# Performance work log

Hardware: AMD Instinct MI355X
Metric: run time of the kernel (lower is better)

## Reference

```python
import jax, jax.numpy as jnp
import numpy as np

N, NFEAT, NHID, NREL, NCLASS, NHEADS = 4096, 512, 64, 64, 16, 8
ALPHA = 0.2   # LeakyReLU negative slope
NEG = -9e15   # pyGAT mask value


def _gat_layer(x, rel, mask, adj_ad, W, a1, a2, concat):
    # x: [N, Fin], rel: [nrel, Fin], mask: [N, N] bool, adj_ad: [N, nrel]
    xr = x + adj_ad @ rel                 # relation-augmented node features
    h = xr @ W                            # [N, Fout]
    f1 = h @ a1                           # [N]  (a^T[Wh_i||Wh_j] = f1_i + f2_j)
    f2 = h @ a2                           # [N]
    e = jax.nn.leaky_relu(f1[:, None] + f2[None, :], ALPHA)  # [N, N]
    att = jax.nn.softmax(jnp.where(mask, e, NEG), axis=1)
    out = att @ h                         # [N, Fout]
    return jax.nn.elu(out) if concat else out


def setup_inputs() -> dict:
    key = jax.random.key(0)
    ks = jax.random.split(key, 12)
    x = jax.random.normal(ks[0], (N, NFEAT), jnp.float32)
    rel = jax.random.normal(ks[1], (NREL, NFEAT), jnp.float32)
    rel_dict = jax.random.randint(ks[2], (N,), 0, NREL, jnp.int32)
    adj = (jax.random.uniform(ks[3], (N, N)) < 0.01).astype(jnp.float32)
    adj = jnp.maximum(adj, jnp.eye(N, dtype=jnp.float32))  # self loops
    adj_ad = jax.random.uniform(ks[4], (N, NREL), jnp.float32)
    adj_ad = adj_ad / adj_ad.sum(axis=1, keepdims=True)
    s_in = 1.0 / np.sqrt(NFEAT)
    s_hid = 1.0 / np.sqrt(NHID)
    s_cat = 1.0 / np.sqrt(NHID * NHEADS)
    W_heads = jax.random.normal(ks[5], (NHEADS, NFEAT, NHID), jnp.float32) * s_in
    a1_heads = jax.random.normal(ks[6], (NHEADS, NHID), jnp.float32) * s_hid
    a2_heads = jax.random.normal(ks[7], (NHEADS, NHID), jnp.float32) * s_hid
    W_out = jax.random.normal(ks[8], (NHID * NHEADS, NFEAT), jnp.float32) * s_cat
    a1_out = jax.random.normal(ks[9], (NFEAT,), jnp.float32) * s_in
    a2_out = jax.random.normal(ks[10], (NFEAT,), jnp.float32) * s_in
    lin_W = jax.random.normal(ks[11], (NFEAT, NCLASS), jnp.float32) * s_in
    lin_b = jnp.zeros((NCLASS,), jnp.float32)
    return {"x": x, "rel": rel, "rel_dict": rel_dict, "adj": adj, "adj_ad": adj_ad,
            "W_heads": W_heads, "a1_heads": a1_heads, "a2_heads": a2_heads,
            "W_out": W_out, "a1_out": a1_out, "a2_out": a2_out,
            "lin_W": lin_W, "lin_b": lin_b}


def reference(x, rel, rel_dict, adj, adj_ad, W_heads, a1_heads, a2_heads,
              W_out, a1_out, a2_out, lin_W, lin_b):
    # dropout is identity at inference (training=False); rel_dict is only used
    # by the repo to build adj/adj_ad, so it is a non-math constant here.
    mask = adj > 0
    # multi-head GAT layer, heads fused via vmap then concatenated on feature dim
    heads = jax.vmap(lambda W, a1, a2: _gat_layer(x, rel, mask, adj_ad, W, a1, a2, True))(
        W_heads, a1_heads, a2_heads)                      # [H, N, NHID]
    hcat = jnp.moveaxis(heads, 0, 1).reshape(N, NHEADS * NHID)  # [N, H*NHID]
    h2 = _gat_layer(hcat, rel, mask, adj_ad, W_out, a1_out, a2_out, False)  # [N, NFEAT]
    logits = jax.nn.elu(h2 @ lin_W + lin_b)               # [N, NCLASS]
    return jax.nn.log_softmax(logits, axis=1)
```

## Files before the change

### kernel.cpp

```cpp
#include <hip/hip_runtime.h>

#define NN      4096
#define FEAT    512
#define KDIM    576
#define NHID    64
#define NHEADS  8
#define NCLS    16
#define MAXDEG  128
#define ALPHA   0.2f

typedef __bf16 bf16_t;
typedef __bf16 bf16x8_t __attribute__((ext_vector_type(8)));
typedef float  f32x4_t  __attribute__((ext_vector_type(4)));
typedef unsigned short us8_t __attribute__((ext_vector_type(8)));

__device__ inline unsigned short f2bf(float f) {
    unsigned int u = __float_as_uint(f);
    u += 0x7fffu + ((u >> 16) & 1u);
    return (unsigned short)(u >> 16);
}
__device__ inline float bfu2f(unsigned short b) {
    return __uint_as_float(((unsigned int)b) << 16);
}
__device__ inline void gload16(const void* g, void* s) {
    __builtin_amdgcn_global_load_lds(
        (const __attribute__((address_space(1))) void*)g,
        (__attribute__((address_space(3))) void*)s, 16, 0, 0);
}

#define PREP_REL0   0
#define PREP_TR0    256
#define PREP_Z0     384
#define PREP_CAST0  520
#define PREP_CSR0   2568
#define PREP_NBLK   3592

__global__ __launch_bounds__(256) void prep_kernel(
    const float* __restrict__ adj, int* __restrict__ deg, int* __restrict__ cols,
    const float* __restrict__ adj_ad, const float* __restrict__ rel,
    const float* __restrict__ x, bf16_t* __restrict__ Abf,
    bf16_t* __restrict__ Abf2,
    const float* __restrict__ Wh, const float* __restrict__ Wo,
    unsigned short* __restrict__ WcT, unsigned short* __restrict__ WoT,
    float* __restrict__ fzero) {
    int b = blockIdx.x;
    int t = threadIdx.x;
    __shared__ float smem[64 * 65];
    if (b < PREP_TR0) {
        int r  = b & 63;
        int nh = (b >> 6) & 1;
        int n  = nh * 256 + t;
        smem[t]       = rel[r * FEAT + t];
        smem[t + 256] = rel[r * FEAT + 256 + t];
        __syncthreads();
        float acc[8] = {};
        if (b < 128) {
            int h = n >> 6, f = n & 63;
            const float* p = Wh + (size_t)h * 32768 + f;
            for (int k0 = 0; k0 < 512; k0 += 8)
                #pragma unroll
                for (int u = 0; u < 8; ++u)
                    acc[u] += smem[k0 + u] * p[(size_t)(k0 + u) * 64];
            float s = ((acc[0] + acc[1]) + (acc[2] + acc[3]))
                    + ((acc[4] + acc[5]) + (acc[6] + acc[7]));
            WcT[(size_t)n * KDIM + 512 + r] = f2bf(s);
        } else {
            const float* p = Wo + n;
            for (int k0 = 0; k0 < 512; k0 += 8)
                #pragma unroll
                for (int u = 0; u < 8; ++u)
                    acc[u] += smem[k0 + u] * p[(size_t)(k0 + u) * 512];
            float s = ((acc[0] + acc[1]) + (acc[2] + acc[3]))
                    + ((acc[4] + acc[5]) + (acc[6] + acc[7]));
            WoT[(size_t)n * KDIM + 512 + r] = f2bf(s);
        }
    } else if (b < PREP_Z0) {
        int tb = b - PREP_TR0;
        if (tb < 64) {
            int h = tb >> 3, k0 = (tb & 7) * 64;
            const float* src = Wh + (size_t)h * 32768 + (size_t)k0 * 64;
            #pragma unroll
            for (int i2 = 0; i2 < 16; ++i2) {
                int li = t + i2 * 256;
                float v = src[li];
                smem[(li & 63) * 65 + (li >> 6)] = v;
            }
            __syncthreads();
            #pragma unroll
            for (int i2 = 0; i2 < 16; ++i2) {
                int li = t + i2 * 256;
                int f = li >> 6, r = li & 63;
                WcT[(size_t)(h * 64 + f) * KDIM + k0 + r] = f2bf(smem[f * 65 + r]);
            }
        } else {
            int wb = tb - 64;
            int n0 = (wb & 7) * 64, k0 = (wb >> 3) * 64;
            #pragma unroll
            for (int i2 = 0; i2 < 16; ++i2) {
                int li = t + i2 * 256;
                int r = li >> 6, f = li & 63;
                float v = Wo[(size_t)(k0 + r) * 512 + n0 + f];
                smem[f * 65 + r] = v;
            }
            __syncthreads();
            #pragma unroll
            for (int i2 = 0; i2 < 16; ++i2) {
                int li = t + i2 * 256;
                int f = li >> 6, r = li & 63;
                WoT[(size_t)(n0 + f) * KDIM + k0 + r] = f2bf(smem[f * 65 + r]);
            }
        }
    } else if (b < PREP_CAST0) {
        int g = (b - PREP_Z0) * 256 + t;
        ((float4*)fzero)[g] = make_float4(0.f, 0.f, 0.f, 0.f);
    } else if (b < PREP_CSR0) {
        int half = t >> 7;
        int tt = t & 127;
        size_t i = (size_t)(b - PREP_CAST0) * 2 + half;
        float4 xv = ((const float4*)(x + i * FEAT))[tt];
        ushort4 o;
        o.x = f2bf(xv.x); o.y = f2bf(xv.y);
        o.z = f2bf(xv.z); o.w = f2bf(xv.w);
        *(ushort4*)(Abf + i * KDIM + 4 * tt) = o;
        if (tt < 16) {
            float4 av = ((const float4*)(adj_ad + i * 64))[tt];
            ushort4 o2;
            o2.x = f2bf(av.x); o2.y = f2bf(av.y);
            o2.z = f2bf(av.z); o2.w = f2bf(av.w);
            *(ushort4*)(Abf  + i * KDIM + 512 + 4 * tt) = o2;
            *(ushort4*)(Abf2 + i * KDIM + 512 + 4 * tt) = o2;
        }
    } else {
        int l = t & 63;
        int i = (b - PREP_CSR0) * 4 + (t >> 6);
        const float4* row4 = (const float4*)(adj + (size_t)i * NN);
        float4 v[16];
        #pragma unroll
        for (int c2 = 0; c2 < 16; ++c2) v[c2] = row4[l + c2 * 64];
        unsigned long long mask = 0;
        #pragma unroll
        for (int c2 = 0; c2 < 16; ++c2) {
            unsigned m4 = (unsigned)(v[c2].x > 0.0f)
                        | ((unsigned)(v[c2].y > 0.0f) << 1)
                        | ((unsigned)(v[c2].z > 0.0f) << 2)
                        | ((unsigned)(v[c2].w > 0.0f) << 3);
            mask |= (unsigned long long)m4 << (4 * c2);
        }
        int c = __popcll(mask);
        int pre = c;
        #pragma unroll
        for (int off = 1; off < 64; off <<= 1) {
            int n = __shfl_up(pre, off);
            if (l >= off) pre += n;
        }
        int base = pre - c;
        if (l == 63) deg[i] = pre > MAXDEG ? MAXDEG : pre;
        int* colrow = cols + i * MAXDEG;
        int idx = base;
        while (mask) {
            int bit = (int)__ffsll(mask) - 1;
            mask &= mask - 1;
            int j = 4 * l + ((bit >> 2) << 8) + (bit & 3);
            if (idx < MAXDEG) colrow[idx] = j;
            ++idx;
        }
    }
}

__global__ __launch_bounds__(256) void gemm_bf16_dot_kernel(
    const bf16_t* __restrict__ A, const bf16_t* __restrict__ Bt,
    unsigned short* __restrict__ Cbf,
    const float* __restrict__ a1, const float* __restrict__ a2,
    float* __restrict__ f1, float* __restrict__ f2, int layer2,
    const float* __restrict__ linW, float* __restrict__ G) {
    __shared__ __align__(16) bf16_t ABs[2][64][64];
    float* Ct = (float*)ABs;
    const int bm = blockIdx.x * 64;
    const int bn = blockIdx.y * 64;
    const int by = blockIdx.y;
    const int t  = threadIdx.x;
    const int l  = t & 63;
    const int w  = t >> 6;
    const int wr = w >> 1;
    const int wc = w & 1;
    const int c16 = l & 15;
    const int q8  = (l >> 4) * 8;
    const int r4  = (l >> 4) * 4;

    const bf16_t* Abase = A  + (size_t)bm * KDIM;
    const bf16_t* Bbase = Bt + (size_t)bn * KDIM;

    f32x4_t acc[2][2] = {};
    for (int k0 = 0; k0 < KDIM; k0 += 64) {
        #pragma unroll
        for (int c = 0; c < 2; ++c) {
            int cb = c * 256 + w * 64;
            int li = cb + l;
            int r = li >> 3, pc = li & 7;
            int lc = pc ^ (r & 7);
            gload16(Abase + (size_t)r * KDIM + k0 + lc * 8,
                    (char*)&ABs[0][0][0] + cb * 16);
        }
        #pragma unroll
        for (int c = 0; c < 2; ++c) {
            int cb = c * 256 + w * 64;
            int li = cb + l;
            int r = li >> 3, pc = li & 7;
            int lc = pc ^ (r & 7);
            gload16(Bbase + (size_t)r * KDIM + k0 + lc * 8,
                    (char*)&ABs[1][0][0] + cb * 16);
        }
        __syncthreads();
        #pragma unroll
        for (int kk = 0; kk < 64; kk += 32) {
            const int ck = (kk + q8) >> 3;
            bf16x8_t af[2], bfr[2];
            #pragma unroll
            for (int mi = 0; mi < 2; ++mi) {
                int R = wr * 32 + mi * 16 + c16;
                af[mi] = *(const bf16x8_t*)&ABs[0][R][(ck ^ (R & 7)) * 8];
            }
            #pragma unroll
            for (int ni = 0; ni < 2; ++ni) {
                int R = wc * 32 + ni * 16 + c16;
                bfr[ni] = *(const bf16x8_t*)&ABs[1][R][(ck ^ (R & 7)) * 8];
            }
            #pragma unroll
            for (int mi = 0; mi < 2; ++mi)
                #pragma unroll
                for (int ni = 0; ni < 2; ++ni)
                    acc[mi][ni] = __builtin_amdgcn_mfma_f32_16x16x32_bf16(
                        af[mi], bfr[ni], acc[mi][ni], 0, 0, 0);
        }
        __syncthreads();
    }
    if (layer2) {
        #pragma unroll
        for (int mi = 0; mi < 2; ++mi)
            #pragma unroll
            for (int ni = 0; ni < 2; ++ni)
                #pragma unroll
                for (int r = 0; r < 4; ++r)
                    Ct[(wr * 32 + mi * 16 + r4 + r) * 64
                       + wc * 32 + ni * 16 + c16] = acc[mi][ni][r];
    }
    #pragma unroll
    for (int mi = 0; mi < 2; ++mi)
        #pragma unroll
        for (int ni = 0; ni < 2; ++ni)
            #pragma unroll
            for (int r = 0; r < 4; ++r)
                Cbf[(size_t)(bm + wr * 32 + mi * 16 + r4 + r) * FEAT
                    + bn + wc * 32 + ni * 16 + c16] = f2bf(acc[mi][ni][r]);

    float a1v[2], a2v[2];
    #pragma unroll
    for (int ni = 0; ni < 2; ++ni) {
        a1v[ni] = a1[bn + wc * 32 + ni * 16 + c16];
        a2v[ni] = a2[bn + wc * 32 + ni * 16 + c16];
    }
    float p1[2][4] = {}, p2[2][4] = {};
    #pragma unroll
    for (int mi = 0; mi < 2; ++mi)
        #pragma unroll
        for (int ni = 0; ni < 2; ++ni)
            #pragma unroll
            for (int r = 0; r < 4; ++r) {
                p1[mi][r] += acc[mi][ni][r] * a1v[ni];
                p2[mi][r] += acc[mi][ni][r] * a2v[ni];
            }
    #pragma unroll
    for (int off = 1; off <= 8; off <<= 1)
        #pragma unroll
        for (int mi = 0; mi < 2; ++mi)
            #pragma unroll
            for (int r = 0; r < 4; ++r) {
                p1[mi][r] += __shfl_xor(p1[mi][r], off);
                p2[mi][r] += __shfl_xor(p2[mi][r], off);
            }
    if (c16 == 0) {
        int fbase = layer2 ? 0 : by * NN;
        #pragma unroll
        for (int mi = 0; mi < 2; ++mi)
            #pragma unroll
            for (int r = 0; r < 4; ++r) {
                int row = bm + wr * 32 + mi * 16 + r4 + r;
                atomicAdd(&f1[fbase + row], p1[mi][r]);
                atomicAdd(&f2[fbase + row], p2[mi][r]);
            }
    }
    if (layer2) {
        __syncthreads();
        int row = t >> 2;
        int cls0 = (t & 3) * 4;
        float pg[4] = {};
        #pragma unroll 8
        for (int c = 0; c < 64; ++c) {
            float cv = Ct[row * 64 + c];
            float4 wv = *(const float4*)&linW[(size_t)(bn + c) * NCLS + cls0];
            pg[0] += cv * wv.x; pg[1] += cv * wv.y;
            pg[2] += cv * wv.z; pg[3] += cv * wv.w;
        }
        #pragma unroll
        for (int j = 0; j < 4; ++j)
            atomicAdd(&G[(size_t)(bm + row) * NCLS + cls0 + j], pg[j]);
    }
}

__global__ __launch_bounds__(512) void att1_kernel(
    const bf16_t* __restrict__ Hbf, const float* __restrict__ f1,
    const float* __restrict__ f2, const int* __restrict__ deg,
    const int* __restrict__ cols, bf16_t* __restrict__ outbf) {
    int i = blockIdx.x;
    int tid = threadIdx.x;
    int h = tid >> 6;
    int l = tid & 63;
    __shared__ int jl[MAXDEG];
    __shared__ float se[NHEADS][MAXDEG];
    __shared__ float part[NHEADS][FEAT];
    __shared__ float sinv[NHEADS];
    __shared__ int sdeg;
    if (tid == 0) sdeg = deg[i];
    __syncthreads();
    int d = sdeg;
    int dpad = (d + 31) & ~31;
    for (int k = tid; k < dpad; k += 512)
        jl[k] = (k < d) ? cols[i * MAXDEG + k] : i;
    __syncthreads();
    float fi = f1[h * NN + i];
    float lmax = -1e30f;
    for (int k = l; k < d; k += 64) {
        float e = fi + f2[h * NN + jl[k]];
        e = e > 0.0f ? e : ALPHA * e;
        se[h][k] = e;
        lmax = fmaxf(lmax, e);
    }
    for (int off = 32; off; off >>= 1) lmax = fmaxf(lmax, __shfl_down(lmax, off));
    float m = __shfl(lmax, 0);
    float ls = 0.0f;
    for (int k = l; k < d; k += 64) {
        float p = __expf(se[h][k] - m);
        se[h][k] = p;
        ls += p;
    }
    for (int k = d + l; k < dpad; k += 64) se[h][k] = 0.0f;
    for (int off = 32; off; off >>= 1) ls += __shfl_down(ls, off);
    if (l == 0) sinv[h] = 1.0f / ls;
    __syncthreads();
    const int myhead = l >> 3;
    float acc[8] = {};
    for (int k0 = 0; k0 < dpad; k0 += 32) {
        float pw[4];
        const bf16_t* rp[4];
        #pragma unroll
        for (int j = 0; j < 4; ++j) {
            int k = k0 + j * 8 + h;
            pw[j] = se[myhead][k];
            rp[j] = Hbf + (size_t)jl[k] * FEAT + l * 8;
        }
        #pragma unroll
        for (int j = 0; j < 4; ++j) {
            us8_t v = *(const us8_t*)rp[j];
            float p = pw[j];
            #pragma unroll
            for (int q = 0; q < 8; ++q) acc[q] += p * bfu2f(v[q]);
        }
    }
    *(float4*)&part[h][l * 8]     = make_float4(acc[0], acc[1], acc[2], acc[3]);
    *(float4*)&part[h][l * 8 + 4] = make_float4(acc[4], acc[5], acc[6], acc[7]);
    __syncthreads();
    {
        float sum = 0.0f;
        #pragma unroll
        for (int w2 = 0; w2 < NHEADS; ++w2) sum += part[w2][tid];
        float o = sum * sinv[tid >> 6];
        o = o > 0.0f ? o : __expf(o) - 1.0f;
        ((unsigned short*)outbf)[(size_t)i * KDIM + tid] = f2bf(o);
    }
}

__global__ __launch_bounds__(256) void att2_final_kernel(
    const float* __restrict__ G, const float* __restrict__ f1,
    const float* __restrict__ f2, const int* __restrict__ deg,
    const int* __restrict__ cols, const float* __restrict__ linb,
    float* __restrict__ out) {
    int i = blockIdx.x;
    int t = threadIdx.x;
    __shared__ int jl[MAXDEG];
    __shared__ float sp[MAXDEG];
    __shared__ float red[4];
    __shared__ float clsred[16][NCLS];
    __shared__ float sl[NCLS];
    __shared__ int sdeg;
    if (t == 0) sdeg = deg[i];
    __syncthreads();
    int d = sdeg;
    int dpad = (d + 15) & ~15;
    if (t < dpad) jl[t] = (t < d) ? cols[i * MAXDEG + t] : i;
    __syncthreads();
    float e = 0.0f, lmax = -1e30f;
    if (t < d) {
        e = f1[i] + f2[jl[t]];
        e = e > 0.0f ? e : ALPHA * e;
        lmax = e;
    }
    for (int off = 32; off; off >>= 1) lmax = fmaxf(lmax, __shfl_down(lmax, off));
    if ((t & 63) == 0) red[t >> 6] = lmax;
    __syncthreads();
    float m = fmaxf(fmaxf(red[0], red[1]), fmaxf(red[2], red[3]));
    float p = 0.0f;
    if (t < d) p = __expf(e - m);
    if (t < dpad) sp[t] = p;
    float ls = p;
    for (int off = 32; off; off >>= 1) ls += __shfl_down(ls, off);
    __syncthreads();
    if ((t & 63) == 0) red[t >> 6] = ls;
    __syncthreads();
    float s = red[0] + red[1] + red[2] + red[3];
    float inv = 1.0f / s;
    {
        int slot = t >> 4;
        int cls  = t & 15;
        float fa[4] = {};
        for (int k = slot; k < dpad; k += 16)
            fa[(k >> 4) & 3] += sp[k] * G[(size_t)jl[k] * NCLS + cls];
        clsred[slot][cls] = (fa[0] + fa[1]) + (fa[2] + fa[3]);
    }
    __syncthreads();
    if (t < NCLS) {
        float dot = 0.0f;
        #pragma unroll
        for (int seg = 0; seg < 16; ++seg) dot += clsred[seg][t];
        float logit = linb[t] + dot * inv;
        logit = logit > 0.0f ? logit : __expf(logit) - 1.0f;
        sl[t] = logit;
    }
    __syncthreads();
    if (t < NCLS) {
        float mm = sl[0];
        #pragma unroll
        for (int c = 1; c < NCLS; ++c) mm = fmaxf(mm, sl[c]);
        float ssum = 0.0f;
        #pragma unroll
        for (int c = 0; c < NCLS; ++c) ssum += __expf(sl[c] - mm);
        out[i * NCLS + t] = sl[t] - mm - logf(ssum);
    }
}

extern "C" void kernel_launch(void* const* d_in, const int* in_sizes, int n_in,
                              void* d_out, int out_size, void* d_ws, size_t ws_size,
                              hipStream_t stream) {
    const float* x        = (const float*)d_in[0];
    const float* rel      = (const float*)d_in[1];
    const float* adj      = (const float*)d_in[3];
    const float* adj_ad   = (const float*)d_in[4];
    const float* W_heads  = (const float*)d_in[5];
    const float* a1_heads = (const float*)d_in[6];
    const float* a2_heads = (const float*)d_in[7];
    const float* W_out    = (const float*)d_in[8];
    const float* a1_out   = (const float*)d_in[9];
    const float* a2_out   = (const float*)d_in[10];
    const float* lin_W    = (const float*)d_in[11];
    const float* lin_b    = (const float*)d_in[12];
    float* out = (float*)d_out;

    char* ws = (char*)d_ws;
    bf16_t* Abf  = (bf16_t*)(ws);
    bf16_t* Abf2 = (bf16_t*)(ws + (5u  << 20));
    bf16_t* Hbf1 = (bf16_t*)(ws + (10u << 20));
    bf16_t* Hbf2 = (bf16_t*)(ws + (14u << 20));
    bf16_t* WcT  = (bf16_t*)(ws + (18u << 20));
    bf16_t* WoT  = (bf16_t*)(ws + (19u << 20));
    float*  f1   = (float*) (ws + (20u << 20));
    float*  f2   = (float*) (ws + (20u << 20) + (128u << 10));
    float*  f1o  = (float*) (ws + (20u << 20) + (256u << 10));
    float*  f2o  = (float*) (ws + (20u << 20) + (272u << 10));
    float*  G    = (float*) (ws + (20u << 20) + (288u << 10));
    int*    deg  = (int*)   (ws + (20u << 20) + (544u << 10));
    int*    cols = (int*)   (ws + (21u << 20));

    prep_kernel<<<PREP_NBLK, 256, 0, stream>>>(
        adj, deg, cols, adj_ad, rel, x, Abf, Abf2, W_heads, W_out,
        (unsigned short*)WcT, (unsigned short*)WoT, f1);
    gemm_bf16_dot_kernel<<<dim3(64, 8), 256, 0, stream>>>(
        Abf, WcT, (unsigned short*)Hbf1, a1_heads, a2_heads, f1, f2, 0,
        nullptr, nullptr);
    att1_kernel<<<NN, 512, 0, stream>>>(Hbf1, f1, f2, deg, cols, Abf2);
    gemm_bf16_dot_kernel<<<dim3(64, 8), 256, 0, stream>>>(
        Abf2, WoT, (unsigned short*)Hbf2, a1_out, a2_out, f1o, f2o, 1,
        lin_W, G);
    att2_final_kernel<<<NN, 256, 0, stream>>>(G, f1o, f2o, deg, cols, lin_b, out);
}
```

Measured before the change: 188.3 us.

## Fuse adjacency CSR construction into first attention kernel

Moves the dense adjacency scan that builds neighbor lists from the prep kernel into att1_kernel. Each attention block now reads its own adjacency row, builds the column list straight into shared memory with a two-level prefix scan, and writes deg/cols out for the later att2 kernel. This removes the global cols reads in att1 and shrinks prep's grid, but it puts the 64 MB adjacency read on att1's critical path and adds a block-wide sync at the start of att1. Column ordering changes from a per-wave interleaved layout to a per-thread-strided one, so neighbors end up in a different order.

Result: no change. 188.6 us (+0.2%).

```diff
diff --git a/kernel.cpp b/kernel.cpp
--- a/kernel.cpp
+++ b/kernel.cpp
@@ -32,11 +32,9 @@
 #define PREP_TR0    256
 #define PREP_Z0     384
 #define PREP_CAST0  520
-#define PREP_CSR0   2568
-#define PREP_NBLK   3592
+#define PREP_NBLK   2568
 
 __global__ __launch_bounds__(256) void prep_kernel(
-    const float* __restrict__ adj, int* __restrict__ deg, int* __restrict__ cols,
     const float* __restrict__ adj_ad, const float* __restrict__ rel,
     const float* __restrict__ x, bf16_t* __restrict__ Abf,
     bf16_t* __restrict__ Abf2,
@@ -113,7 +111,7 @@
     } else if (b < PREP_CAST0) {
         int g = (b - PREP_Z0) * 256 + t;
         ((float4*)fzero)[g] = make_float4(0.f, 0.f, 0.f, 0.f);
-    } else if (b < PREP_CSR0) {
+    } else {
         int half = t >> 7;
         int tt = t & 127;
         size_t i = (size_t)(b - PREP_CAST0) * 2 + half;
@@ -129,40 +127,6 @@
             o2.z = f2bf(av.z); o2.w = f2bf(av.w);
             *(ushort4*)(Abf  + i * KDIM + 512 + 4 * tt) = o2;
             *(ushort4*)(Abf2 + i * KDIM + 512 + 4 * tt) = o2;
-        }
-    } else {
-        int l = t & 63;
-        int i = (b - PREP_CSR0) * 4 + (t >> 6);
-        const float4* row4 = (const float4*)(adj + (size_t)i * NN);
-        float4 v[16];
-        #pragma unroll
-        for (int c2 = 0; c2 < 16; ++c2) v[c2] = row4[l + c2 * 64];
-        unsigned long long mask = 0;
-        #pragma unroll
-        for (int c2 = 0; c2 < 16; ++c2) {
-            unsigned m4 = (unsigned)(v[c2].x > 0.0f)
-                        | ((unsigned)(v[c2].y > 0.0f) << 1)
-                        | ((unsigned)(v[c2].z > 0.0f) << 2)
-                        | ((unsigned)(v[c2].w > 0.0f) << 3);
-            mask |= (unsigned long long)m4 << (4 * c2);
-        }
-        int c = __popcll(mask);
-        int pre = c;
-        #pragma unroll
-        for (int off = 1; off < 64; off <<= 1) {
-            int n = __shfl_up(pre, off);
-            if (l >= off) pre += n;
-        }
-        int base = pre - c;
-        if (l == 63) deg[i] = pre > MAXDEG ? MAXDEG : pre;
-        int* colrow = cols + i * MAXDEG;
-        int idx = base;
-        while (mask) {
-            int bit = (int)__ffsll(mask) - 1;
-            mask &= mask - 1;
-            int j = 4 * l + ((bit >> 2) << 8) + (bit & 3);
-            if (idx < MAXDEG) colrow[idx] = j;
-            ++idx;
         }
     }
 }
@@ -308,9 +272,9 @@
 }
 
 __global__ __launch_bounds__(512) void att1_kernel(
+    const float* __restrict__ adj, int* __restrict__ deg, int* __restrict__ cols,
     const bf16_t* __restrict__ Hbf, const float* __restrict__ f1,
-    const float* __restrict__ f2, const int* __restrict__ deg,
-    const int* __restrict__ cols, bf16_t* __restrict__ outbf) {
+    const float* __restrict__ f2, bf16_t* __restrict__ outbf) {
     int i = blockIdx.x;
     int tid = threadIdx.x;
     int h = tid >> 6;
@@ -319,14 +283,53 @@
     __shared__ float se[NHEADS][MAXDEG];
     __shared__ float part[NHEADS][FEAT];
     __shared__ float sinv[NHEADS];
+    __shared__ int wsum[8];
     __shared__ int sdeg;
-    if (tid == 0) sdeg = deg[i];
+    {
+        const float4* row4 = (const float4*)(adj + (size_t)i * NN);
+        float4 v0 = row4[tid];
+        float4 v1 = row4[tid + 512];
+        unsigned m = 0;
+        m |= (unsigned)(v0.x > 0.0f) << 0;  m |= (unsigned)(v0.y > 0.0f) << 1;
+        m |= (unsigned)(v0.z > 0.0f) << 2;  m |= (unsigned)(v0.w > 0.0f) << 3;
+        m |= (unsigned)(v1.x > 0.0f) << 4;  m |= (unsigned)(v1.y > 0.0f) << 5;
+        m |= (unsigned)(v1.z > 0.0f) << 6;  m |= (unsigned)(v1.w > 0.0f) << 7;
+        int c = __popc(m);
+        int pre = c;
+        #pragma unroll
+        for (int off = 1; off < 64; off <<= 1) {
+            int n = __shfl_up(pre, off);
+            if (l >= off) pre += n;
+        }
+        if (l == 63) wsum[h] = pre;
+        __syncthreads();
+        int base = pre - c;
+        #pragma unroll
+        for (int w2 = 0; w2 < 8; ++w2)
+            if (w2 < h) base += wsum[w2];
+        unsigned mm = m;
+        int idx = base;
+        while (mm) {
+            int bit = __ffs(mm) - 1;
+            mm &= mm - 1;
+            int j = 4 * tid + ((bit >> 2) << 11) + (bit & 3);
+            if (idx < MAXDEG) jl[idx] = j;
+            ++idx;
+        }
+        if (tid == 0) {
+            int tot = 0;
+            #pragma unroll
+            for (int w2 = 0; w2 < 8; ++w2) tot += wsum[w2];
+            tot = tot > MAXDEG ? MAXDEG : tot;
+            sdeg = tot;
+            deg[i] = tot;
+        }
+    }
     __syncthreads();
     int d = sdeg;
     int dpad = (d + 31) & ~31;
-    for (int k = tid; k < dpad; k += 512)
-        jl[k] = (k < d) ? cols[i * MAXDEG + k] : i;
-    __syncthreads();
+    for (int k = d + tid; k < dpad; k += 512) jl[k] = i;
+    for (int k = tid; k < d; k += 512) cols[i * MAXDEG + k] = jl[k];
     float fi = f1[h * NN + i];
     float lmax = -1e30f;
     for (int k = l; k < d; k += 64) {
@@ -480,12 +483,13 @@
     int*    cols = (int*)   (ws + (21u << 20));
 
     prep_kernel<<<PREP_NBLK, 256, 0, stream>>>(
-        adj, deg, cols, adj_ad, rel, x, Abf, Abf2, W_heads, W_out,
+        adj_ad, rel, x, Abf, Abf2, W_heads, W_out,
         (unsigned short*)WcT, (unsigned short*)WoT, f1);
     gemm_bf16_dot_kernel<<<dim3(64, 8), 256, 0, stream>>>(
         Abf, WcT, (unsigned short*)Hbf1, a1_heads, a2_heads, f1, f2, 0,
         nullptr, nullptr);
-    att1_kernel<<<NN, 512, 0, stream>>>(Hbf1, f1, f2, deg, cols, Abf2);
+    att1_kernel<<<NN, 512, 0, stream>>>(
+        adj, deg, cols, Hbf1, f1, f2, Abf2);
     gemm_bf16_dot_kernel<<<dim3(64, 8), 256, 0, stream>>>(
         Abf2, WoT, (unsigned short*)Hbf2, a1_out, a2_out, f1o, f2o, 1,
         lin_W, G);
```

## Move adjacency CSR build from prep kernel into first GEMM launch

Applied to the files above, without the earlier changes.

The dense-adjacency-to-CSR scan (reading the 64MB fp32 adj) moves out of the prep kernel and into extra blocks appended to the first GEMM launch, so the memory-bound scan can overlap with the compute-bound GEMM blocks. The GEMM grid becomes 1D with a manual block-index decode. The layer-2 GEMM also stops writing the unused bf16 H output. This makes the prep kernel shorter, at the cost of a more heterogeneous GEMM launch whose CSR blocks may compete with GEMM blocks for bandwidth and CUs.

Result: slower. 192.6 us (+2.3%).

```diff
diff --git a/kernel.cpp b/kernel.cpp
--- a/kernel.cpp
+++ b/kernel.cpp
@@ -9,6 +9,8 @@
 #define MAXDEG  128
 #define ALPHA   0.2f
 
+#define GEMM_BLKS 512
+
 typedef __bf16 bf16_t;
 typedef __bf16 bf16x8_t __attribute__((ext_vector_type(8)));
 typedef float  f32x4_t  __attribute__((ext_vector_type(4)));
@@ -32,11 +34,9 @@
 #define PREP_TR0    256
 #define PREP_Z0     384
 #define PREP_CAST0  520
-#define PREP_CSR0   2568
-#define PREP_NBLK   3592
+#define PREP_NBLK   2568
 
 __global__ __launch_bounds__(256) void prep_kernel(
-    const float* __restrict__ adj, int* __restrict__ deg, int* __restrict__ cols,
     const float* __restrict__ adj_ad, const float* __restrict__ rel,
     const float* __restrict__ x, bf16_t* __restrict__ Abf,
     bf16_t* __restrict__ Abf2,
@@ -113,7 +113,7 @@
     } else if (b < PREP_CAST0) {
         int g = (b - PREP_Z0) * 256 + t;
         ((float4*)fzero)[g] = make_float4(0.f, 0.f, 0.f, 0.f);
-    } else if (b < PREP_CSR0) {
+    } else {
         int half = t >> 7;
         int tt = t & 127;
         size_t i = (size_t)(b - PREP_CAST0) * 2 + half;
@@ -130,9 +130,22 @@
             *(ushort4*)(Abf  + i * KDIM + 512 + 4 * tt) = o2;
             *(ushort4*)(Abf2 + i * KDIM + 512 + 4 * tt) = o2;
         }
-    } else {
+    }
+}
+
+__global__ __launch_bounds__(256) void gemm_bf16_dot_kernel(
+    const bf16_t* __restrict__ A, const bf16_t* __restrict__ Bt,
+    unsigned short* __restrict__ Cbf,
+    const float* __restrict__ a1, const float* __restrict__ a2,
+    float* __restrict__ f1, float* __restrict__ f2, int layer2,
+    const float* __restrict__ linW, float* __restrict__ G,
+    const float* __restrict__ adj, int* __restrict__ deg,
+    int* __restrict__ cols) {
+    const int bid = blockIdx.x;
+    const int t   = threadIdx.x;
+    if (bid >= GEMM_BLKS) {
         int l = t & 63;
-        int i = (b - PREP_CSR0) * 4 + (t >> 6);
+        int i = (bid - GEMM_BLKS) * 4 + (t >> 6);
         const float4* row4 = (const float4*)(adj + (size_t)i * NN);
         float4 v[16];
         #pragma unroll
@@ -164,21 +177,13 @@
             if (idx < MAXDEG) colrow[idx] = j;
             ++idx;
         }
-    }
-}
-
-__global__ __launch_bounds__(256) void gemm_bf16_dot_kernel(
-    const bf16_t* __restrict__ A, const bf16_t* __restrict__ Bt,
-    unsigned short* __restrict__ Cbf,
-    const float* __restrict__ a1, const float* __restrict__ a2,
-    float* __restrict__ f1, float* __restrict__ f2, int layer2,
-    const float* __restrict__ linW, float* __restrict__ G) {
+        return;
+    }
     __shared__ __align__(16) bf16_t ABs[2][64][64];
     float* Ct = (float*)ABs;
-    const int bm = blockIdx.x * 64;
-    const int bn = blockIdx.y * 64;
-    const int by = blockIdx.y;
-    const int t  = threadIdx.x;
+    const int bm = (bid >> 3) * 64;
+    const int by = bid & 7;
+    const int bn = by * 64;
     const int l  = t & 63;
     const int w  = t >> 6;
     const int wr = w >> 1;
@@ -243,15 +248,16 @@
                 for (int r = 0; r < 4; ++r)
                     Ct[(wr * 32 + mi * 16 + r4 + r) * 64
                        + wc * 32 + ni * 16 + c16] = acc[mi][ni][r];
-    }
-    #pragma unroll
-    for (int mi = 0; mi < 2; ++mi)
-        #pragma unroll
-        for (int ni = 0; ni < 2; ++ni)
-            #pragma unroll
-            for (int r = 0; r < 4; ++r)
-                Cbf[(size_t)(bm + wr * 32 + mi * 16 + r4 + r) * FEAT
-                    + bn + wc * 32 + ni * 16 + c16] = f2bf(acc[mi][ni][r]);
+    } else {
+        #pragma unroll
+        for (int mi = 0; mi < 2; ++mi)
+            #pragma unroll
+            for (int ni = 0; ni < 2; ++ni)
+                #pragma unroll
+                for (int r = 0; r < 4; ++r)
+                    Cbf[(size_t)(bm + wr * 32 + mi * 16 + r4 + r) * FEAT
+                        + bn + wc * 32 + ni * 16 + c16] = f2bf(acc[mi][ni][r]);
+    }
 
     float a1v[2], a2v[2];
     #pragma unroll
@@ -480,14 +486,14 @@
     int*    cols = (int*)   (ws + (21u << 20));
 
     prep_kernel<<<PREP_NBLK, 256, 0, stream>>>(
-        adj, deg, cols, adj_ad, rel, x, Abf, Abf2, W_heads, W_out,
+        adj_ad, rel, x, Abf, Abf2, W_heads, W_out,
         (unsigned short*)WcT, (unsigned short*)WoT, f1);
-    gemm_bf16_dot_kernel<<<dim3(64, 8), 256, 0, stream>>>(
+    gemm_bf16_dot_kernel<<<GEMM_BLKS + 1024, 256, 0, stream>>>(
         Abf, WcT, (unsigned short*)Hbf1, a1_heads, a2_heads, f1, f2, 0,
-        nullptr, nullptr);
+        nullptr, nullptr, adj, deg, cols);
     att1_kernel<<<NN, 512, 0, stream>>>(Hbf1, f1, f2, deg, cols, Abf2);
-    gemm_bf16_dot_kernel<<<dim3(64, 8), 256, 0, stream>>>(
+    gemm_bf16_dot_kernel<<<GEMM_BLKS, 256, 0, stream>>>(
         Abf2, WoT, (unsigned short*)Hbf2, a1_out, a2_out, f1o, f2o, 1,
-        lin_W, G);
+        lin_W, G, nullptr, nullptr, nullptr);
     att2_final_kernel<<<NN, 256, 0, stream>>>(G, f1o, f2o, deg, cols, lin_b, out);
 }
```
